# Kernel tuning notes

Hardware: AMD Instinct MI355X
Metric: run time of the kernel (lower is better)

The kernel has to match this reference:

```python
import jax, jax.numpy as jnp
import numpy as np

B, C, H, W = 64, 256, 32, 32
HID = C // 16          # SE hidden = channels // ratio
EMB = 16               # channel/snr embed dim
COND = 2 * EMB         # cond vector dim = 32
RHID = 64              # rate controller hidden
SNR_DB = 10.0
CH_IDX = 2             # 'Combined_channel'
POWER = 2.0
BASE_CR, MIN_CR, MAX_CR, ALPHA = 0.5, 0.3, 1.0, 0.7


def setup_inputs() -> dict:
    key = jax.random.key(0)
    ks = jax.random.split(key, 16)
    g = lambda k, sh: (jax.random.normal(k, sh, dtype=jnp.float32) * 0.05)
    return {
        "x": jax.random.normal(ks[0], (B, C, H, W), dtype=jnp.float32),
        "channel_embed": g(ks[1], (3, EMB)),
        "snr_w1": g(ks[2], (EMB, 1)), "snr_b1": jnp.zeros((EMB,), jnp.float32),
        "snr_w2": g(ks[3], (EMB, EMB)), "snr_b2": jnp.zeros((EMB,), jnp.float32),
        "base_w1": g(ks[4], (HID, C)),
        "base_w2": g(ks[5], (C, HID)),
        "sem_proj": g(ks[6], (HID, C)),
        "cond_proj": g(ks[7], (HID, COND)),
        "out_proj": g(ks[8], (C, HID)),
        "r_w1": g(ks[9], (RHID, C + COND)), "r_b1": jnp.zeros((RHID,), jnp.float32),
        "r_w2": g(ks[10], (RHID, RHID)), "r_b2": jnp.zeros((RHID,), jnp.float32),
        "r_w3": g(ks[11], (1, RHID)), "r_b3": jnp.zeros((1,), jnp.float32),
    }


def _topk_mask(weights, k):
    # weights [B,C], k [B] int; keep top-k per row (vectorized rank trick).
    order = jnp.argsort(-weights, axis=1)
    ranks = jnp.argsort(order, axis=1)
    return (ranks < k[:, None]).astype(weights.dtype)


def reference(x, channel_embed, snr_w1, snr_b1, snr_w2, snr_b2,
              base_w1, base_w2, sem_proj, cond_proj, out_proj,
              r_w1, r_b1, r_w2, r_b2, r_w3, r_b3):
    b, c, h, w = x.shape
    sem = x.mean(axis=(2, 3))                                   # [B,C] GAP
    # channel condition encoder
    ch_vec = jnp.broadcast_to(channel_embed[CH_IDX], (b, EMB))
    s_in = jnp.full((b, 1), SNR_DB / 28.0, dtype=x.dtype)
    sv = jax.nn.relu(s_in @ snr_w1.T + snr_b1)
    sv = jax.nn.relu(sv @ snr_w2.T + snr_b2)
    cond = jnp.concatenate([ch_vec, sv], axis=1)                # [B,32]
    # base SE weights * channel-conditioned gate
    base = jax.nn.sigmoid(jax.nn.relu(sem @ base_w1.T) @ base_w2.T)
    gate = jax.nn.sigmoid(jax.nn.relu(sem @ sem_proj.T + cond @ cond_proj.T) @ out_proj.T)
    weights = base * gate                                       # [B,C]
    # rate controller -> per-sample cr
    r = jax.nn.relu(jnp.concatenate([sem, cond], axis=1) @ r_w1.T + r_b1)
    r = jax.nn.relu(r @ r_w2.T + r_b2)
    raw = jax.nn.sigmoid(r @ r_w3.T + r_b3)[:, 0]
    dyn = MIN_CR + (MAX_CR - MIN_CR) * raw
    cr = jnp.clip((1.0 - ALPHA) * BASE_CR + ALPHA * dyn, MIN_CR, MAX_CR)
    k = jnp.clip(jnp.round(cr * c).astype(jnp.int32), 1, c)
    mask = _topk_mask(weights, k)
    z = x * (weights * mask)[:, :, None, None]                  # masked latent
    # --- combined channel: flat Rayleigh fading + per-(b,c,h) AWGN ---
    F = c * h * w
    zf = z.reshape(b, F)
    xr, xi = zf[:, 0::2], zf[:, 1::2]                           # [B,F/2]
    nk = jax.random.split(jax.random.key(42), 5)
    hr = jax.random.normal(nk[0], xr.shape, x.dtype)            # torch h_i (real)
    hi = jax.random.normal(nk[1], xr.shape, x.dtype)            # torch h_r (imag)
    std = jnp.sqrt(jnp.asarray(POWER / (10.0 ** (SNR_DB / 10.0)), x.dtype))
    nr = std * jax.random.normal(nk[2], xr.shape, x.dtype)
    ni = std * jax.random.normal(nk[3], xr.shape, x.dtype)
    yr = hr * xr - hi * xi + nr
    yi = hr * xi + hi * xr + ni
    den = hr * hr + hi * hi
    outr = (yr * hr + yi * hi) / den
    outi = (yi * hr - yr * hi) / den
    faded = jnp.stack([outr, outi], axis=-1).reshape(b, c, h, w)
    # per-(b,c,h) random SNR map AWGN
    kk = jax.random.split(nk[4], 2)
    snr_map = jax.random.randint(kk[0], (b, c, h, 1), 0, 29).astype(x.dtype)
    std2 = jnp.sqrt(POWER / (10.0 ** (snr_map / 10.0)))
    return faded + std2 * jax.random.normal(kk[1], (b, c, h, w), x.dtype)
```

## Files before the change

### kernel.cpp

```cpp
#include <hip/hip_runtime.h>

#define NB 64
#define NC 256
#define NF 262144
#define NROWS 524288

struct U2 { unsigned a, b; };

__host__ __device__ constexpr unsigned rotl32(unsigned x, int d) {
  return (x << d) | (x >> (32 - d));
}

__host__ __device__ constexpr U2 tf2x32(unsigned k0, unsigned k1,
                                        unsigned x0, unsigned x1) {
  const unsigned ks0 = k0, ks1 = k1, ks2 = k0 ^ k1 ^ 0x1BD11BDAu;
  x0 += ks0; x1 += ks1;
  x0 += x1; x1 = rotl32(x1, 13); x1 ^= x0;
  x0 += x1; x1 = rotl32(x1, 15); x1 ^= x0;
  x0 += x1; x1 = rotl32(x1, 26); x1 ^= x0;
  x0 += x1; x1 = rotl32(x1, 6);  x1 ^= x0;
  x0 += ks1; x1 += ks2 + 1u;
  x0 += x1; x1 = rotl32(x1, 17); x1 ^= x0;
  x0 += x1; x1 = rotl32(x1, 29); x1 ^= x0;
  x0 += x1; x1 = rotl32(x1, 16); x1 ^= x0;
  x0 += x1; x1 = rotl32(x1, 24); x1 ^= x0;
  x0 += ks2; x1 += ks0 + 2u;
  x0 += x1; x1 = rotl32(x1, 13); x1 ^= x0;
  x0 += x1; x1 = rotl32(x1, 15); x1 ^= x0;
  x0 += x1; x1 = rotl32(x1, 26); x1 ^= x0;
  x0 += x1; x1 = rotl32(x1, 6);  x1 ^= x0;
  x0 += ks0; x1 += ks1 + 3u;
  x0 += x1; x1 = rotl32(x1, 17); x1 ^= x0;
  x0 += x1; x1 = rotl32(x1, 29); x1 ^= x0;
  x0 += x1; x1 = rotl32(x1, 16); x1 ^= x0;
  x0 += x1; x1 = rotl32(x1, 24); x1 ^= x0;
  x0 += ks1; x1 += ks2 + 4u;
  x0 += x1; x1 = rotl32(x1, 13); x1 ^= x0;
  x0 += x1; x1 = rotl32(x1, 15); x1 ^= x0;
  x0 += x1; x1 = rotl32(x1, 26); x1 ^= x0;
  x0 += x1; x1 = rotl32(x1, 6);  x1 ^= x0;
  x0 += ks2; x1 += ks0 + 5u;
  return U2{x0, x1};
}

constexpr U2 NK0 = tf2x32(0u, 42u, 0u, 0u);
constexpr U2 NK1 = tf2x32(0u, 42u, 0u, 1u);
constexpr U2 NK2 = tf2x32(0u, 42u, 0u, 2u);
constexpr U2 NK3 = tf2x32(0u, 42u, 0u, 3u);
constexpr U2 NK4 = tf2x32(0u, 42u, 0u, 4u);
constexpr U2 KK0 = tf2x32(NK4.a, NK4.b, 0u, 0u);
constexpr U2 KK1 = tf2x32(NK4.a, NK4.b, 0u, 1u);

__device__ __forceinline__ unsigned rb32(unsigned k0, unsigned k1, unsigned m) {
  const unsigned ks2 = k0 ^ k1 ^ 0x1BD11BDAu;
  unsigned x0 = k0, x1 = m + k1;
#define QR(r) x0 += x1; x1 = __builtin_rotateleft32(x1, r); x1 ^= x0;
  QR(13) QR(15) QR(26) QR(6)
  x0 += k1;  x1 += ks2 + 1u;
  QR(17) QR(29) QR(16) QR(24)
  x0 += ks2; x1 += k0 + 2u;
  QR(13) QR(15) QR(26) QR(6)
  x0 += k0;  x1 += k1 + 3u;
  QR(17) QR(29) QR(16) QR(24)
  x0 += k1;  x1 += ks2 + 4u;
  QR(13) QR(15) QR(26) QR(6)
  x0 += ks2; x1 += k0 + 5u;
#undef QR
  return x0 ^ x1;
}

template <int S>
__device__ __forceinline__ float normal_fast(unsigned bits) {
  constexpr float K = (S == 0) ? 1.41421356f : 1.41421356f * 0.44721359f;
  const float lo = __uint_as_float(0xBF7FFFFFu);
  float u = __uint_as_float((bits >> 9) | 0x3F800000u) - 1.0f;
  float v = fmaf(u, 2.0f, lo);
  float t = fmaf(-v, v, 1.0f);
  float L = __builtin_amdgcn_logf(t);
  float p;
  if (L > -7.2134752f) {
    float z = fmaf(L, -0.69314718f, -2.5f);
    p = K * 2.81022636e-08f;
    p = fmaf(p, z, K * 3.43273939e-07f);
    p = fmaf(p, z, K * -3.5233877e-06f);
    p = fmaf(p, z, K * -4.39150654e-06f);
    p = fmaf(p, z, K * 0.00021858087f);
    p = fmaf(p, z, K * -0.00125372503f);
    p = fmaf(p, z, K * -0.00417768164f);
    p = fmaf(p, z, K * 0.246640727f);
    p = fmaf(p, z, K * 1.50140941f);
  } else {
    float w = L * -0.69314718f;
    float z = __builtin_amdgcn_sqrtf(w) - 3.0f;
    p = K * -0.000200214257f;
    p = fmaf(p, z, K * 0.000100950558f);
    p = fmaf(p, z, K * 0.00134934322f);
    p = fmaf(p, z, K * -0.00367342844f);
    p = fmaf(p, z, K * 0.00573950773f);
    p = fmaf(p, z, K * -0.0076224613f);
    p = fmaf(p, z, K * 0.00943887047f);
    p = fmaf(p, z, K * 1.00167406f);
    p = fmaf(p, z, K * 2.83297682f);
  }
  return p * v;
}

__global__ __launch_bounds__(256) void prep_kernel(const float* __restrict__ x,
                                                   float* __restrict__ sem,
                                                   float* __restrict__ std2) {
  if (blockIdx.x < 4096) {
    int row = (blockIdx.x * 256 + threadIdx.x) >> 6;
    int lane = threadIdx.x & 63;
    const float* rp = x + (size_t)row * 1024;
    float acc = 0.0f;
#pragma unroll
    for (int i = 0; i < 4; ++i) {
      float4 v = *(const float4*)(rp + i * 256 + lane * 4);
      acc += v.x + v.y + v.z + v.w;
    }
#pragma unroll
    for (int off = 32; off > 0; off >>= 1) acc += __shfl_down(acc, off, 64);
    if (lane == 0) sem[row] = acc * (1.0f / 1024.0f);
  } else {
    const unsigned j = (blockIdx.x - 4096u) * 256u + threadIdx.x;
    unsigned hb = rb32(KK0.a, KK0.b, j);
    unsigned lb = rb32(KK0.a, KK0.b, NROWS + j);
    unsigned snr = ((hb % 29u) * 16u + (lb % 29u)) % 29u;
    std2[j] = __builtin_amdgcn_sqrtf(
        2.0f * __builtin_amdgcn_exp2f((float)snr * -0.33219281f));
  }
}

__global__ __launch_bounds__(256) void head_kernel(
    const float* __restrict__ sem_g, const float* __restrict__ channel_embed,
    const float* __restrict__ snr_w1, const float* __restrict__ snr_b1,
    const float* __restrict__ snr_w2, const float* __restrict__ snr_b2,
    const float* __restrict__ base_w1, const float* __restrict__ base_w2,
    const float* __restrict__ sem_proj, const float* __restrict__ cond_proj,
    const float* __restrict__ out_proj, const float* __restrict__ r_w1,
    const float* __restrict__ r_b1, const float* __restrict__ r_w2,
    const float* __restrict__ r_b2, const float* __restrict__ r_w3,
    const float* __restrict__ r_b3, float* __restrict__ s_out) {
  __shared__ float conc_s[288];
  __shared__ float sv1_s[16];
  __shared__ float hid_s[16], g1_s[16];
  __shared__ float r1_s[64], r2_s[64];
  __shared__ float w_s[256];
  __shared__ int k_s;
  const int b = blockIdx.x, t = threadIdx.x;
  const int wv = t >> 6, ln = t & 63;

  conc_s[t] = sem_g[b * 256 + t];
  if (t < 16) {
    const float s_in = (float)(10.0 / 28.0);
    sv1_s[t] = fmaxf(0.0f, s_in * snr_w1[t] + snr_b1[t]);
  }
  __syncthreads();
  if (t < 16) {
    float a = snr_b2[t];
    for (int f = 0; f < 16; ++f) a += sv1_s[f] * snr_w2[t * 16 + f];
    conc_s[272 + t] = fmaxf(0.0f, a);
    conc_s[256 + t] = channel_embed[32 + t];
  }
  __syncthreads();

  for (int j = wv; j < 96; j += 4) {
    float acc = 0.0f;
    if (j < 16) {
#pragma unroll
      for (int k = 0; k < 4; ++k)
        acc += base_w1[j * 256 + ln + k * 64] * conc_s[ln + k * 64];
    } else if (j < 32) {
      int r = j - 16;
#pragma unroll
      for (int k = 0; k < 4; ++k)
        acc += sem_proj[r * 256 + ln + k * 64] * conc_s[ln + k * 64];
      if (ln < 32) acc += cond_proj[r * 32 + ln] * conc_s[256 + ln];
    } else {
      int r = j - 32;
#pragma unroll
      for (int k = 0; k < 4; ++k)
        acc += r_w1[r * 288 + ln + k * 64] * conc_s[ln + k * 64];
      if (ln < 32) acc += r_w1[r * 288 + 256 + ln] * conc_s[256 + ln];
    }
#pragma unroll
    for (int off = 32; off > 0; off >>= 1) acc += __shfl_xor(acc, off, 64);
    if (ln == 0) {
      if (j < 16) hid_s[j] = fmaxf(0.0f, acc);
      else if (j < 32) g1_s[j - 16] = fmaxf(0.0f, acc);
      else r1_s[j - 32] = fmaxf(0.0f, acc + r_b1[j - 32]);
    }
  }
  __syncthreads();

  if (t < 64) {
    float a = r_b2[t];
    for (int j = 0; j < 64; ++j) a += r1_s[j] * r_w2[t * 64 + j];
    r2_s[t] = fmaxf(0.0f, a);
  }
  {
    float a1 = 0.0f, a2 = 0.0f;
#pragma unroll
    for (int i = 0; i < 16; ++i) {
      a1 += hid_s[i] * base_w2[t * 16 + i];
      a2 += g1_s[i] * out_proj[t * 16 + i];
    }
    float base = 1.0f / (1.0f + expf(-a1));
    float gate = 1.0f / (1.0f + expf(-a2));
    w_s[t] = base * gate;
  }
  __syncthreads();
  if (t == 0) {
    float a = r_b3[0];
    for (int j = 0; j < 64; ++j) a += r2_s[j] * r_w3[j];
    float raw = 1.0f / (1.0f + expf(-a));
    float dyn = 0.3f + 0.7f * raw;
    float cr = 0.15f + 0.7f * dyn;
    cr = fminf(fmaxf(cr, 0.3f), 1.0f);
    int k = (int)rintf(cr * 256.0f);
    k_s = min(max(k, 1), 256);
  }
  __syncthreads();
  {
    float wc = w_s[t];
    int cnt = 0;
    for (int j = 0; j < 256; ++j) {
      float wj = w_s[j];
      cnt += (wj > wc) || (wj == wc && j < t);
    }
    s_out[b * 256 + t] = (cnt < k_s) ? wc : 0.0f;
  }
}

__global__ __launch_bounds__(256) void sim_kernel(const float* __restrict__ x,
                                                  const float* __restrict__ s,
                                                  const float* __restrict__ std2v,
                                                  float* __restrict__ out) {
  const unsigned tid = blockIdx.x * 256u + threadIdx.x;
  const unsigned q0 = tid * 8u;

  const float4 xa = *(const float4*)(x + q0);
  const float4 xb = *(const float4*)(x + q0 + 4);
  const float sc = s[q0 >> 10];
  const float std2 = std2v[q0 >> 5];

  const unsigned m0 = tid * 4u;
  float hr[4], hi[4], nr[4], ni[4], n2[8];
#pragma unroll
  for (int i = 0; i < 4; ++i)
    hr[i] = normal_fast<0>(rb32(NK0.a, NK0.b, m0 + i));
#pragma unroll
  for (int i = 0; i < 4; ++i)
    hi[i] = normal_fast<0>(rb32(NK1.a, NK1.b, m0 + i));
#pragma unroll
  for (int i = 0; i < 4; ++i)
    nr[i] = normal_fast<1>(rb32(NK2.a, NK2.b, m0 + i));
#pragma unroll
  for (int i = 0; i < 4; ++i)
    ni[i] = normal_fast<1>(rb32(NK3.a, NK3.b, m0 + i));
#pragma unroll
  for (int i = 0; i < 8; ++i)
    n2[i] = normal_fast<0>(rb32(KK1.a, KK1.b, q0 + i));

  float xs[8] = {xa.x * sc, xa.y * sc, xa.z * sc, xa.w * sc,
                 xb.x * sc, xb.y * sc, xb.z * sc, xb.w * sc};
  float o[8];
#pragma unroll
  for (int i = 0; i < 4; ++i) {
    const float den = fmaf(hr[i], hr[i], hi[i] * hi[i]);
    const float rc = __builtin_amdgcn_rcpf(den);
    o[2 * i] = fmaf(fmaf(hr[i], nr[i], hi[i] * ni[i]), rc, xs[2 * i]);
    o[2 * i + 1] =
        fmaf(fmaf(hr[i], ni[i], -(hi[i] * nr[i])), rc, xs[2 * i + 1]);
  }
  float4 oa, ob;
  oa.x = fmaf(std2, n2[0], o[0]);
  oa.y = fmaf(std2, n2[1], o[1]);
  oa.z = fmaf(std2, n2[2], o[2]);
  oa.w = fmaf(std2, n2[3], o[3]);
  ob.x = fmaf(std2, n2[4], o[4]);
  ob.y = fmaf(std2, n2[5], o[5]);
  ob.z = fmaf(std2, n2[6], o[6]);
  ob.w = fmaf(std2, n2[7], o[7]);
  *(float4*)(out + q0) = oa;
  *(float4*)(out + q0 + 4) = ob;
}

extern "C" void kernel_launch(void* const* d_in, const int* in_sizes, int n_in,
                              void* d_out, int out_size, void* d_ws,
                              size_t ws_size, hipStream_t stream) {
  const float* x = (const float*)d_in[0];
  const float* channel_embed = (const float*)d_in[1];
  const float* snr_w1 = (const float*)d_in[2];
  const float* snr_b1 = (const float*)d_in[3];
  const float* snr_w2 = (const float*)d_in[4];
  const float* snr_b2 = (const float*)d_in[5];
  const float* base_w1 = (const float*)d_in[6];
  const float* base_w2 = (const float*)d_in[7];
  const float* sem_proj = (const float*)d_in[8];
  const float* cond_proj = (const float*)d_in[9];
  const float* out_proj = (const float*)d_in[10];
  const float* r_w1 = (const float*)d_in[11];
  const float* r_b1 = (const float*)d_in[12];
  const float* r_w2 = (const float*)d_in[13];
  const float* r_b2 = (const float*)d_in[14];
  const float* r_w3 = (const float*)d_in[15];
  const float* r_b3 = (const float*)d_in[16];

  float* std2 = (float*)d_ws;
  float* sem = std2 + NROWS;
  float* s = sem + NB * NC;

  prep_kernel<<<4096 + NROWS / 256, 256, 0, stream>>>(x, sem, std2);
  head_kernel<<<NB, 256, 0, stream>>>(sem, channel_embed, snr_w1, snr_b1,
                                      snr_w2, snr_b2, base_w1, base_w2,
                                      sem_proj, cond_proj, out_proj, r_w1,
                                      r_b1, r_w2, r_b2, r_w3, r_b3, s);
  sim_kernel<<<NB * NF / 8 / 256, 256, 0, stream>>>(x, s, std2, (float*)d_out);
}
```

Measured before the change: 140.6 us.

## Precompute per-element AWGN noise in fp16 during prep, simplify head GEMVs

The per-element second AWGN term (std2 times a normal draw) is now generated in the prep kernel, alongside the GAP reduction, and stored as fp16 in workspace. The sim kernel reads this buffer instead of computing those random numbers itself. This moves RNG work off the critical sim pass so it can overlap with the memory-bound mean reduction, at the cost of an extra 32 MB fp16 write and read and reduced noise precision. The head kernel's matvecs are also rewritten from wave-per-row shuffle reductions to one thread per output row with serial loops.

New measurement: 128.3 us. -8.8%, faster.

```diff
diff --git a/kernel.cpp b/kernel.cpp
--- a/kernel.cpp
+++ b/kernel.cpp
@@ -1,4 +1,5 @@
 #include <hip/hip_runtime.h>
+#include <hip/hip_fp16.h>
 
 #define NB 64
 #define NC 256
@@ -105,11 +106,56 @@
   return p * v;
 }
 
+__device__ __forceinline__ float std2_of_row(unsigned j) {
+  unsigned hb = rb32(KK0.a, KK0.b, j);
+  unsigned lb = rb32(KK0.a, KK0.b, NROWS + j);
+  unsigned snr = ((hb % 29u) * 16u + (lb % 29u)) % 29u;
+  return __builtin_amdgcn_sqrtf(
+      2.0f * __builtin_amdgcn_exp2f((float)snr * -0.33219281f));
+}
+
+__global__ __launch_bounds__(256) void prep2_kernel(const float* __restrict__ x,
+                                                    float* __restrict__ sem,
+                                                    __half* __restrict__ noise2) {
+  if (blockIdx.x < 2048) {
+    const unsigned j = blockIdx.x * 256u + threadIdx.x;
+    const float std2 = std2_of_row(j);
+    const unsigned q = j * 32u;
+#pragma unroll
+    for (int cc = 0; cc < 4; ++cc) {
+      union { __half2 h2[4]; uint4 u; } pk;
+#pragma unroll
+      for (int e = 0; e < 4; ++e) {
+        float a = std2 * normal_fast<0>(rb32(KK1.a, KK1.b, q + cc * 8u + 2 * e));
+        float b = std2 * normal_fast<0>(rb32(KK1.a, KK1.b, q + cc * 8u + 2 * e + 1));
+        pk.h2[e] = __floats2half2_rn(a, b);
+      }
+      *(uint4*)(noise2 + q + cc * 8u) = pk.u;
+    }
+  } else {
+    int row = ((blockIdx.x - 2048) * 256 + threadIdx.x) >> 6;
+    int lane = threadIdx.x & 63;
+    const float* rp = x + (size_t)row * 1024;
+    float acc = 0.0f;
+#pragma unroll
+    for (int i = 0; i < 4; ++i) {
+      float4 v = *(const float4*)(rp + i * 256 + lane * 4);
+      acc += v.x + v.y + v.z + v.w;
+    }
+#pragma unroll
+    for (int off = 32; off > 0; off >>= 1) acc += __shfl_down(acc, off, 64);
+    if (lane == 0) sem[row] = acc * (1.0f / 1024.0f);
+  }
+}
+
 __global__ __launch_bounds__(256) void prep_kernel(const float* __restrict__ x,
                                                    float* __restrict__ sem,
                                                    float* __restrict__ std2) {
-  if (blockIdx.x < 4096) {
-    int row = (blockIdx.x * 256 + threadIdx.x) >> 6;
+  if (blockIdx.x < 2048) {
+    const unsigned j = blockIdx.x * 256u + threadIdx.x;
+    std2[j] = std2_of_row(j);
+  } else {
+    int row = ((blockIdx.x - 2048) * 256 + threadIdx.x) >> 6;
     int lane = threadIdx.x & 63;
     const float* rp = x + (size_t)row * 1024;
     float acc = 0.0f;
@@ -121,13 +167,6 @@
 #pragma unroll
     for (int off = 32; off > 0; off >>= 1) acc += __shfl_down(acc, off, 64);
     if (lane == 0) sem[row] = acc * (1.0f / 1024.0f);
-  } else {
-    const unsigned j = (blockIdx.x - 4096u) * 256u + threadIdx.x;
-    unsigned hb = rb32(KK0.a, KK0.b, j);
-    unsigned lb = rb32(KK0.a, KK0.b, NROWS + j);
-    unsigned snr = ((hb % 29u) * 16u + (lb % 29u)) % 29u;
-    std2[j] = __builtin_amdgcn_sqrtf(
-        2.0f * __builtin_amdgcn_exp2f((float)snr * -0.33219281f));
   }
 }
 
@@ -141,16 +180,16 @@
     const float* __restrict__ r_b1, const float* __restrict__ r_w2,
     const float* __restrict__ r_b2, const float* __restrict__ r_w3,
     const float* __restrict__ r_b3, float* __restrict__ s_out) {
-  __shared__ float conc_s[288];
+  __shared__ float sem_s[256];
   __shared__ float sv1_s[16];
+  __shared__ float cond_s[32];
   __shared__ float hid_s[16], g1_s[16];
   __shared__ float r1_s[64], r2_s[64];
   __shared__ float w_s[256];
   __shared__ int k_s;
   const int b = blockIdx.x, t = threadIdx.x;
-  const int wv = t >> 6, ln = t & 63;
-
-  conc_s[t] = sem_g[b * 256 + t];
+
+  sem_s[t] = sem_g[b * 256 + t];
   if (t < 16) {
     const float s_in = (float)(10.0 / 28.0);
     sv1_s[t] = fmaxf(0.0f, s_in * snr_w1[t] + snr_b1[t]);
@@ -159,40 +198,28 @@
   if (t < 16) {
     float a = snr_b2[t];
     for (int f = 0; f < 16; ++f) a += sv1_s[f] * snr_w2[t * 16 + f];
-    conc_s[272 + t] = fmaxf(0.0f, a);
-    conc_s[256 + t] = channel_embed[32 + t];
+    cond_s[16 + t] = fmaxf(0.0f, a);
+    cond_s[t] = channel_embed[2 * 16 + t];
   }
   __syncthreads();
-
-  for (int j = wv; j < 96; j += 4) {
-    float acc = 0.0f;
-    if (j < 16) {
-#pragma unroll
-      for (int k = 0; k < 4; ++k)
-        acc += base_w1[j * 256 + ln + k * 64] * conc_s[ln + k * 64];
-    } else if (j < 32) {
-      int r = j - 16;
-#pragma unroll
-      for (int k = 0; k < 4; ++k)
-        acc += sem_proj[r * 256 + ln + k * 64] * conc_s[ln + k * 64];
-      if (ln < 32) acc += cond_proj[r * 32 + ln] * conc_s[256 + ln];
-    } else {
-      int r = j - 32;
-#pragma unroll
-      for (int k = 0; k < 4; ++k)
-        acc += r_w1[r * 288 + ln + k * 64] * conc_s[ln + k * 64];
-      if (ln < 32) acc += r_w1[r * 288 + 256 + ln] * conc_s[256 + ln];
-    }
-#pragma unroll
-    for (int off = 32; off > 0; off >>= 1) acc += __shfl_xor(acc, off, 64);
-    if (ln == 0) {
-      if (j < 16) hid_s[j] = fmaxf(0.0f, acc);
-      else if (j < 32) g1_s[j - 16] = fmaxf(0.0f, acc);
-      else r1_s[j - 32] = fmaxf(0.0f, acc + r_b1[j - 32]);
-    }
+  if (t < 16) {
+    float a1 = 0.0f, a2 = 0.0f;
+    for (int c = 0; c < 256; ++c) {
+      float sc = sem_s[c];
+      a1 += sc * base_w1[t * 256 + c];
+      a2 += sc * sem_proj[t * 256 + c];
+    }
+    for (int j = 0; j < 32; ++j) a2 += cond_s[j] * cond_proj[t * 32 + j];
+    hid_s[t] = fmaxf(0.0f, a1);
+    g1_s[t] = fmaxf(0.0f, a2);
+  } else if (t < 80) {
+    int i = t - 16;
+    float a = r_b1[i];
+    for (int c = 0; c < 256; ++c) a += sem_s[c] * r_w1[i * 288 + c];
+    for (int j = 0; j < 32; ++j) a += cond_s[j] * r_w1[i * 288 + 256 + j];
+    r1_s[i] = fmaxf(0.0f, a);
   }
   __syncthreads();
-
   if (t < 64) {
     float a = r_b2[t];
     for (int j = 0; j < 64; ++j) a += r1_s[j] * r_w2[t * 64 + j];
@@ -200,7 +227,6 @@
   }
   {
     float a1 = 0.0f, a2 = 0.0f;
-#pragma unroll
     for (int i = 0; i < 16; ++i) {
       a1 += hid_s[i] * base_w2[t * 16 + i];
       a2 += g1_s[i] * out_proj[t * 16 + i];
@@ -230,6 +256,58 @@
     }
     s_out[b * 256 + t] = (cnt < k_s) ? wc : 0.0f;
   }
+}
+
+__global__ __launch_bounds__(256) void sim2_kernel(
+    const float* __restrict__ x, const float* __restrict__ s,
+    const __half* __restrict__ noise2, float* __restrict__ out) {
+  const unsigned tid = blockIdx.x * 256u + threadIdx.x;
+  const unsigned q0 = tid * 8u;
+
+  const float4 xa = *(const float4*)(x + q0);
+  const float4 xb = *(const float4*)(x + q0 + 4);
+  const uint4 nbits = *(const uint4*)(noise2 + q0);
+  const float sc = s[q0 >> 10];
+
+  const unsigned m0 = tid * 4u;
+  float hr[4], hi[4], nr[4], ni[4];
+#pragma unroll
+  for (int i = 0; i < 4; ++i)
+    hr[i] = normal_fast<0>(rb32(NK0.a, NK0.b, m0 + i));
+#pragma unroll
+  for (int i = 0; i < 4; ++i)
+    hi[i] = normal_fast<0>(rb32(NK1.a, NK1.b, m0 + i));
+#pragma unroll
+  for (int i = 0; i < 4; ++i)
+    nr[i] = normal_fast<1>(rb32(NK2.a, NK2.b, m0 + i));
+#pragma unroll
+  for (int i = 0; i < 4; ++i)
+    ni[i] = normal_fast<1>(rb32(NK3.a, NK3.b, m0 + i));
+
+  union { uint4 u; __half2 h2[4]; } pk; pk.u = nbits;
+  const float2 f01 = __half22float2(pk.h2[0]);
+  const float2 f23 = __half22float2(pk.h2[1]);
+  const float2 f45 = __half22float2(pk.h2[2]);
+  const float2 f67 = __half22float2(pk.h2[3]);
+
+  float xs[8] = {xa.x * sc, xa.y * sc, xa.z * sc, xa.w * sc,
+                 xb.x * sc, xb.y * sc, xb.z * sc, xb.w * sc};
+  float o[8];
+#pragma unroll
+  for (int i = 0; i < 4; ++i) {
+    const float den = fmaf(hr[i], hr[i], hi[i] * hi[i]);
+    const float rc = __builtin_amdgcn_rcpf(den);
+    o[2 * i] = fmaf(fmaf(hr[i], nr[i], hi[i] * ni[i]), rc, xs[2 * i]);
+    o[2 * i + 1] =
+        fmaf(fmaf(hr[i], ni[i], -(hi[i] * nr[i])), rc, xs[2 * i + 1]);
+  }
+  float4 oa, ob;
+  oa.x = o[0] + f01.x; oa.y = o[1] + f01.y;
+  oa.z = o[2] + f23.x; oa.w = o[3] + f23.y;
+  ob.x = o[4] + f45.x; ob.y = o[5] + f45.y;
+  ob.z = o[6] + f67.x; ob.w = o[7] + f67.y;
+  *(float4*)(out + q0) = oa;
+  *(float4*)(out + q0 + 4) = ob;
 }
 
 __global__ __launch_bounds__(256) void sim_kernel(const float* __restrict__ x,
@@ -307,14 +385,28 @@
   const float* r_w3 = (const float*)d_in[15];
   const float* r_b3 = (const float*)d_in[16];
 
-  float* std2 = (float*)d_ws;
-  float* sem = std2 + NROWS;
-  float* s = sem + NB * NC;
-
-  prep_kernel<<<4096 + NROWS / 256, 256, 0, stream>>>(x, sem, std2);
-  head_kernel<<<NB, 256, 0, stream>>>(sem, channel_embed, snr_w1, snr_b1,
-                                      snr_w2, snr_b2, base_w1, base_w2,
-                                      sem_proj, cond_proj, out_proj, r_w1,
-                                      r_b1, r_w2, r_b2, r_w3, r_b3, s);
-  sim_kernel<<<NB * NF / 8 / 256, 256, 0, stream>>>(x, s, std2, (float*)d_out);
-}
+  const size_t need = (size_t)NB * NF * sizeof(__half) + 2u * 16384u * 4u;
+  if (ws_size >= need) {
+    __half* noise2 = (__half*)d_ws;
+    float* sem = (float*)((char*)d_ws + (size_t)NB * NF * sizeof(__half));
+    float* s = sem + NB * NC;
+    prep2_kernel<<<6144, 256, 0, stream>>>(x, sem, noise2);
+    head_kernel<<<NB, 256, 0, stream>>>(sem, channel_embed, snr_w1, snr_b1,
+                                        snr_w2, snr_b2, base_w1, base_w2,
+                                        sem_proj, cond_proj, out_proj, r_w1,
+                                        r_b1, r_w2, r_b2, r_w3, r_b3, s);
+    sim2_kernel<<<NB * NF / 8 / 256, 256, 0, stream>>>(x, s, noise2,
+                                                       (float*)d_out);
+  } else {
+    float* std2 = (float*)d_ws;
+    float* sem = std2 + NROWS;
+    float* s = sem + NB * NC;
+    prep_kernel<<<6144, 256, 0, stream>>>(x, sem, std2);
+    head_kernel<<<NB, 256, 0, stream>>>(sem, channel_embed, snr_w1, snr_b1,
+                                        snr_w2, snr_b2, base_w1, base_w2,
+                                        sem_proj, cond_proj, out_proj, r_w1,
+                                        r_b1, r_w2, r_b2, r_w3, r_b3, s);
+    sim_kernel<<<NB * NF / 8 / 256, 256, 0, stream>>>(x, s, std2,
+                                                      (float*)d_out);
+  }
+}
```
